# Performance work log

Measured on AMD Instinct MI355X. Metric: run time of the kernel, lower is better.

## Reference

```python
import jax, jax.numpy as jnp
import numpy as np

EPS = 1e-12


def setup_inputs() -> dict:
    key = jax.random.key(0)
    k1, k2 = jax.random.split(key)
    ide_feats = jax.random.normal(k1, (4096, 256), dtype=jnp.float32)
    u_feats = jax.random.normal(k2, (16384, 256), dtype=jnp.float32)
    return {"ide_feats": ide_feats, "u_feats": u_feats}


def reference(ide_feats, u_feats):
    # euclidean_dist: sqrt(sum((x_i - y_j)^2) + eps) -> [N, M]
    # computed via the GEMM expansion to avoid the [N, M, D] intermediate
    x2 = jnp.sum(ide_feats * ide_feats, axis=-1)[:, None]   # [N, 1]
    y2 = jnp.sum(u_feats * u_feats, axis=-1)[None, :]       # [1, M]
    xy = jnp.einsum('nd,md->nm', ide_feats, u_feats)        # [N, M]
    d2 = jnp.maximum(x2 + y2 - 2.0 * xy, 0.0)
    dists = jnp.sqrt(d2 + EPS)                              # [N, M]
    d = jnp.mean(dists, axis=-1)                            # [N]
    # dist_loss: sum_{i,j} sqrt((d_i - d_j)^2 + eps)
    diff = d[:, None] - d[None, :]                          # [N, N]
    loss = jnp.sum(jnp.sqrt(diff * diff + EPS))
    return loss
```

## Files before the change

kernel.cpp:

```cpp
#include <hip/hip_runtime.h>
#include <hip/hip_bf16.h>
#include <cstdint>

#define N_IDE 4096
#define M_U   16384
#define D_DIM 256
#define EPSF  1e-12f
#define INV_M (1.0f / 16384.0f)

#define CGC   512
#define BK    32
#define SB_ELEMS (CGC * BK)

typedef _Float16 f16x8 __attribute__((ext_vector_type(8)));
typedef float    f32x4 __attribute__((ext_vector_type(4)));

__device__ __forceinline__ void gll16(const void* g, void* l) {
  __builtin_amdgcn_global_load_lds(
      (const __attribute__((address_space(1))) void*)(uintptr_t)g,
      (__attribute__((address_space(3))) void*)(uint32_t)(uintptr_t)l,
      16, 0, 0);
}

__device__ __forceinline__ unsigned short f2h_bits(float f) {
  _Float16 h = (_Float16)f;
  return __builtin_bit_cast(unsigned short, h);
}

__global__ __launch_bounds__(256) void k_conv(const float* __restrict__ ide,
                                              const float* __restrict__ u,
                                              unsigned short* __restrict__ Ah,
                                              unsigned short* __restrict__ Bh,
                                              float* __restrict__ x2,
                                              float* __restrict__ y2) {
  int gw = (blockIdx.x * 256 + threadIdx.x) >> 6;
  int l  = threadIdx.x & 63;
  const float4* src;
  ushort4* dst;
  float* nrm;
  if (gw < N_IDE) {
    src = (const float4*)(ide + (size_t)gw * D_DIM);
    dst = (ushort4*)(Ah + (size_t)gw * D_DIM);
    nrm = x2 + gw;
  } else {
    int r = gw - N_IDE;
    src = (const float4*)(u + (size_t)r * D_DIM);
    dst = (ushort4*)(Bh + (size_t)r * D_DIM);
    nrm = y2 + r;
  }
  float4 v = src[l];
  float s = v.x * v.x + v.y * v.y + v.z * v.z + v.w * v.w;
  ushort4 o;
  o.x = f2h_bits(v.x); o.y = f2h_bits(v.y);
  o.z = f2h_bits(v.z); o.w = f2h_bits(v.w);
  dst[l] = o;
#pragma unroll
  for (int m = 1; m <= 32; m <<= 1) s += __shfl_xor(s, m, 64);
  if (l == 0) *nrm = s;
}

__global__ __launch_bounds__(512, 2) void k_gemm(const unsigned short* __restrict__ Ah,
                                                 const unsigned short* __restrict__ Bh,
                                                 const float* __restrict__ x2,
                                                 const float* __restrict__ y2,
                                                 float* __restrict__ partial) {
  __shared__ __align__(16) unsigned short sA[128 * 256];
  __shared__ __align__(16) unsigned short sB[2 * SB_ELEMS];
  __shared__ float rowacc[4][128];

  const int t    = threadIdx.x;
  const int w    = t >> 6;
  const int l    = t & 63;
  const int wm   = w >> 2, wn = w & 3;
  const int lrow = l & 15;
  const int lhi  = l >> 4;
  const int bx   = blockIdx.x;
  const int by   = blockIdx.y;

  rowacc[t >> 7][t & 127] = 0.f;

#pragma unroll
  for (int i = 0; i < 8; ++i) {
    int L = i * 512 + t;
    int row = L >> 5;
    int p = L & 31;
    int c = (p & 24) | ((p & 7) ^ (row & 7));
    gll16(Ah + (size_t)(by * 128 + row) * D_DIM + c * 8,
          sA + (size_t)(i * 512 + w * 64) * 8);
  }

  auto stageB = [&](int s) {
    const int cgi = (s >> 3) * 8 + bx;
    const int kt  = s & 7;
    const unsigned short* src = Bh + (size_t)cgi * CGC * D_DIM + kt * BK;
    unsigned short* dstb = sB + (size_t)(s & 1) * SB_ELEMS;
#pragma unroll
    for (int j = 0; j < 4; ++j) {
      int L = j * 512 + t;
      int row = L >> 2;
      int c = L & 3;
      gll16(src + (size_t)row * D_DIM + c * 8,
            dstb + (size_t)(j * 512 + w * 64) * 8);
    }
  };

  float4 x2v[4];
#pragma unroll
  for (int mi = 0; mi < 4; ++mi)
    x2v[mi] = *(const float4*)&x2[by * 128 + wm * 64 + mi * 16 + lhi * 4];

  stageB(0);
  __syncthreads();

  for (int cg = 0; cg < 4; ++cg) {
    const int cgi = cg * 8 + bx;

    f32x4 acc[4][8];
#pragma unroll
    for (int mi = 0; mi < 4; ++mi)
#pragma unroll
      for (int ni = 0; ni < 8; ++ni)
        acc[mi][ni] = (f32x4){0.f, 0.f, 0.f, 0.f};

    for (int kt = 0; kt < 8; ++kt) {
      const int s = cg * 8 + kt;
      if (s + 1 < 32) stageB(s + 1);

      f16x8 af[4];
#pragma unroll
      for (int mi = 0; mi < 4; ++mi) {
        int arow = wm * 64 + mi * 16 + lrow;
        int lc   = kt * 4 + lhi;
        int pc   = (lc & 24) | ((lc & 7) ^ (lrow & 7));
        af[mi] = *(const f16x8*)(sA + (size_t)arow * 256 + pc * 8);
      }

      const unsigned short* bbuf = sB + (size_t)(s & 1) * SB_ELEMS;
#pragma unroll
      for (int half = 0; half < 2; ++half) {
        f16x8 bf[4];
#pragma unroll
        for (int nj = 0; nj < 4; ++nj) {
          int brow = wn * 128 + (half * 4 + nj) * 16 + lrow;
          bf[nj] = *(const f16x8*)(bbuf + (size_t)brow * BK + lhi * 8);
        }
#pragma unroll
        for (int mi = 0; mi < 4; ++mi)
#pragma unroll
          for (int nj = 0; nj < 4; ++nj)
            acc[mi][half * 4 + nj] =
                __builtin_amdgcn_mfma_f32_16x16x32_f16(af[mi], bf[nj],
                                                       acc[mi][half * 4 + nj], 0, 0, 0);
      }
      __syncthreads();
    }

    float yv[8];
#pragma unroll
    for (int ni = 0; ni < 8; ++ni)
      yv[ni] = y2[cgi * CGC + wn * 128 + ni * 16 + lrow];

#pragma unroll
    for (int mi = 0; mi < 4; ++mi) {
      float xr[4] = {x2v[mi].x, x2v[mi].y, x2v[mi].z, x2v[mi].w};
#pragma unroll
      for (int rr = 0; rr < 4; ++rr) {
        float ssum = 0.f;
#pragma unroll
        for (int ni = 0; ni < 8; ++ni) {
          float d2 = xr[rr] + yv[ni] - 2.0f * acc[mi][ni][rr];
          d2 = fmaxf(d2, 0.0f);
          ssum += __builtin_amdgcn_sqrtf(d2 + EPSF);
        }
        ssum += __shfl_xor(ssum, 1, 64);
        ssum += __shfl_xor(ssum, 2, 64);
        ssum += __shfl_xor(ssum, 4, 64);
        ssum += __shfl_xor(ssum, 8, 64);
        if (lrow == 0)
          rowacc[wn][wm * 64 + mi * 16 + lhi * 4 + rr] += ssum;
      }
    }
  }

  __syncthreads();
  if (t < 128)
    partial[(size_t)bx * N_IDE + by * 128 + t] =
        rowacc[0][t] + rowacc[1][t] + rowacc[2][t] + rowacc[3][t];
}

__global__ __launch_bounds__(256) void k_loss(const float* __restrict__ partial,
                                              float* __restrict__ out) {
  __shared__ float sd[N_IDE];
  __shared__ float wsum[4];
  int t = threadIdx.x;
  for (int k = t; k < N_IDE; k += 256) {
    float s = 0.f;
#pragma unroll
    for (int b = 0; b < 8; ++b) s += partial[(size_t)b * N_IDE + k];
    sd[k] = s;
  }
  __syncthreads();
  int tid = blockIdx.x * 256 + t;
  int i   = tid >> 4;
  int jl  = tid & 15;
  float di = sd[i];
  float s  = 0.f;
  for (int k = 0; k < 256; ++k) {
    float diff = (di - sd[jl + k * 16]) * INV_M;
    s += __builtin_amdgcn_sqrtf(diff * diff + EPSF);
  }
#pragma unroll
  for (int m = 1; m <= 32; m <<= 1) s += __shfl_xor(s, m, 64);
  if ((t & 63) == 0) wsum[t >> 6] = s;
  __syncthreads();
  if (t == 0) atomicAdd(out, wsum[0] + wsum[1] + wsum[2] + wsum[3]);
}

extern "C" void kernel_launch(void* const* d_in, const int* in_sizes, int n_in,
                              void* d_out, int out_size, void* d_ws, size_t ws_size,
                              hipStream_t stream) {
  (void)in_sizes; (void)n_in; (void)out_size; (void)ws_size;
  const float* ide = (const float*)d_in[0];
  const float* u   = (const float*)d_in[1];
  float* out = (float*)d_out;

  char* ws = (char*)d_ws;
  size_t off = 0;
  unsigned short* Ah = (unsigned short*)(ws + off); off += (size_t)N_IDE * D_DIM * 2;
  unsigned short* Bh = (unsigned short*)(ws + off); off += (size_t)M_U  * D_DIM * 2;
  float* x2      = (float*)(ws + off); off += (size_t)N_IDE * 4;
  float* y2      = (float*)(ws + off); off += (size_t)M_U * 4;
  float* partial = (float*)(ws + off); off += (size_t)8 * N_IDE * 4;

  hipMemsetAsync(d_out, 0, sizeof(float), stream);
  k_conv<<<(N_IDE + M_U) / 4, 256, 0, stream>>>(ide, u, Ah, Bh, x2, y2);
  k_gemm<<<dim3(8, 32), 512, 0, stream>>>(Ah, Bh, x2, y2, partial);
  k_loss<<<256, 256, 0, stream>>>(partial, out);
}
```

Baseline: 127.8 us.

## Deepen B-tile pipeline to four buffers with swizzled LDS and register row sums

The GEMM kernel's column chunk shrinks from 512 to 256, and B staging moves from double buffering to a 4-deep ring with three tiles in flight. Explicit vmcnt waits plus raw s_barrier replace __syncthreads, and the B LDS layout gets an XOR swizzle to cut bank conflicts. y2 is preloaded into LDS, and row sums stay in registers and are written as 32 partial slots instead of passing through a shared rowacc. This is meant to hide global load latency, reduce accumulator register pressure and remove LDS reduction traffic. In exchange k_loss must sum four times more partials, and the hand-written waitcnt logic is fragile.

```diff
diff --git a/kernel.cpp b/kernel.cpp
--- a/kernel.cpp
+++ b/kernel.cpp
@@ -8,9 +8,11 @@
 #define EPSF  1e-12f
 #define INV_M (1.0f / 16384.0f)
 
-#define CGC   512
+#define CGC   256
 #define BK    32
 #define SB_ELEMS (CGC * BK)
+#define NBUF  4
+#define NSTEP 64
 
 typedef _Float16 f16x8 __attribute__((ext_vector_type(8)));
 typedef float    f32x4 __attribute__((ext_vector_type(4)));
@@ -65,8 +67,8 @@
                                                  const float* __restrict__ y2,
                                                  float* __restrict__ partial) {
   __shared__ __align__(16) unsigned short sA[128 * 256];
-  __shared__ __align__(16) unsigned short sB[2 * SB_ELEMS];
-  __shared__ float rowacc[4][128];
+  __shared__ __align__(16) unsigned short sB[NBUF * SB_ELEMS];
+  __shared__ __align__(16) float sY[8 * CGC];
 
   const int t    = threadIdx.x;
   const int w    = t >> 6;
@@ -76,8 +78,12 @@
   const int lhi  = l >> 4;
   const int bx   = blockIdx.x;
   const int by   = blockIdx.y;
-
-  rowacc[t >> 7][t & 127] = 0.f;
+  const int pchB = lhi ^ ((lrow >> 1) & 3);
+
+  float4 x2v[4];
+#pragma unroll
+  for (int mi = 0; mi < 4; ++mi)
+    x2v[mi] = *(const float4*)&x2[by * 128 + wm * 64 + mi * 16 + lhi * 4];
 
 #pragma unroll
   for (int i = 0; i < 8; ++i) {
@@ -88,104 +94,116 @@
     gll16(Ah + (size_t)(by * 128 + row) * D_DIM + c * 8,
           sA + (size_t)(i * 512 + w * 64) * 8);
   }
+  gll16(y2 + (size_t)(w * 8 + bx) * CGC + l * 4, sY + w * CGC + l * 4);
+
+  const int r0 = t >> 2,        r1 = (512 + t) >> 2;
+  const int c0 = (t & 3) ^ ((r0 >> 1) & 3);
+  const int c1 = (t & 3) ^ ((r1 >> 1) & 3);
+  const size_t soff0 = (size_t)r0 * D_DIM + c0 * 8;
+  const size_t soff1 = (size_t)r1 * D_DIM + c1 * 8;
 
   auto stageB = [&](int s) {
-    const int cgi = (s >> 3) * 8 + bx;
-    const int kt  = s & 7;
-    const unsigned short* src = Bh + (size_t)cgi * CGC * D_DIM + kt * BK;
-    unsigned short* dstb = sB + (size_t)(s & 1) * SB_ELEMS;
-#pragma unroll
-    for (int j = 0; j < 4; ++j) {
-      int L = j * 512 + t;
-      int row = L >> 2;
-      int c = L & 3;
-      gll16(src + (size_t)row * D_DIM + c * 8,
-            dstb + (size_t)(j * 512 + w * 64) * 8);
+    const unsigned short* src =
+        Bh + (size_t)(((s >> 3) * 8 + bx) * CGC) * D_DIM + (s & 7) * BK;
+    unsigned short* dstb = sB + (size_t)(s & 3) * SB_ELEMS;
+    gll16(src + soff0, dstb + (size_t)(w * 64) * 8);
+    gll16(src + soff1, dstb + (size_t)(512 + w * 64) * 8);
+  };
+
+  stageB(0); stageB(1); stageB(2);
+  asm volatile("s_waitcnt vmcnt(4)" ::: "memory");
+  asm volatile("s_barrier" ::: "memory");
+
+  f32x4 acc[4][4];
+#pragma unroll
+  for (int mi = 0; mi < 4; ++mi)
+#pragma unroll
+    for (int nj = 0; nj < 4; ++nj)
+      acc[mi][nj] = (f32x4){0.f, 0.f, 0.f, 0.f};
+
+  float racc[4][4];
+#pragma unroll
+  for (int mi = 0; mi < 4; ++mi)
+#pragma unroll
+    for (int rr = 0; rr < 4; ++rr)
+      racc[mi][rr] = 0.f;
+
+  for (int s = 0; s < NSTEP; ++s) {
+    const int kt = s & 7;
+    if (s + 3 < NSTEP) stageB(s + 3);
+
+    const int lc = kt * 4 + lhi;
+    const int pc = (lc & 24) | ((lc & 7) ^ (lrow & 7));
+    f16x8 af[4];
+#pragma unroll
+    for (int mi = 0; mi < 4; ++mi)
+      af[mi] = *(const f16x8*)(sA + (size_t)(wm * 64 + mi * 16 + lrow) * 256 + pc * 8);
+
+    const unsigned short* bbuf = sB + (size_t)(s & 3) * SB_ELEMS;
+    f16x8 bf[4];
+#pragma unroll
+    for (int nj = 0; nj < 4; ++nj)
+      bf[nj] = *(const f16x8*)(bbuf + (size_t)(wn * 64 + nj * 16 + lrow) * BK + pchB * 8);
+
+#pragma unroll
+    for (int mi = 0; mi < 4; ++mi)
+#pragma unroll
+      for (int nj = 0; nj < 4; ++nj)
+        acc[mi][nj] = __builtin_amdgcn_mfma_f32_16x16x32_f16(af[mi], bf[nj],
+                                                             acc[mi][nj], 0, 0, 0);
+
+    if (kt == 7) {
+      const int cgl = s >> 3;
+      float yv[4];
+#pragma unroll
+      for (int ni = 0; ni < 4; ++ni)
+        yv[ni] = sY[cgl * CGC + wn * 64 + ni * 16 + lrow];
+#pragma unroll
+      for (int mi = 0; mi < 4; ++mi) {
+        float xr[4] = {x2v[mi].x, x2v[mi].y, x2v[mi].z, x2v[mi].w};
+#pragma unroll
+        for (int rr = 0; rr < 4; ++rr) {
+          float ssum = 0.f;
+#pragma unroll
+          for (int ni = 0; ni < 4; ++ni) {
+            float d2 = xr[rr] + yv[ni] - 2.0f * acc[mi][ni][rr];
+            d2 = fmaxf(d2, 0.0f);
+            ssum += __builtin_amdgcn_sqrtf(d2 + EPSF);
+          }
+          racc[mi][rr] += ssum;
+        }
+      }
+#pragma unroll
+      for (int mi = 0; mi < 4; ++mi)
+#pragma unroll
+        for (int nj = 0; nj < 4; ++nj)
+          acc[mi][nj] = (f32x4){0.f, 0.f, 0.f, 0.f};
     }
-  };
-
-  float4 x2v[4];
-#pragma unroll
-  for (int mi = 0; mi < 4; ++mi)
-    x2v[mi] = *(const float4*)&x2[by * 128 + wm * 64 + mi * 16 + lhi * 4];
-
-  stageB(0);
-  __syncthreads();
-
-  for (int cg = 0; cg < 4; ++cg) {
-    const int cgi = cg * 8 + bx;
-
-    f32x4 acc[4][8];
-#pragma unroll
-    for (int mi = 0; mi < 4; ++mi)
-#pragma unroll
-      for (int ni = 0; ni < 8; ++ni)
-        acc[mi][ni] = (f32x4){0.f, 0.f, 0.f, 0.f};
-
-    for (int kt = 0; kt < 8; ++kt) {
-      const int s = cg * 8 + kt;
-      if (s + 1 < 32) stageB(s + 1);
-
-      f16x8 af[4];
-#pragma unroll
-      for (int mi = 0; mi < 4; ++mi) {
-        int arow = wm * 64 + mi * 16 + lrow;
-        int lc   = kt * 4 + lhi;
-        int pc   = (lc & 24) | ((lc & 7) ^ (lrow & 7));
-        af[mi] = *(const f16x8*)(sA + (size_t)arow * 256 + pc * 8);
-      }
-
-      const unsigned short* bbuf = sB + (size_t)(s & 1) * SB_ELEMS;
-#pragma unroll
-      for (int half = 0; half < 2; ++half) {
-        f16x8 bf[4];
-#pragma unroll
-        for (int nj = 0; nj < 4; ++nj) {
-          int brow = wn * 128 + (half * 4 + nj) * 16 + lrow;
-          bf[nj] = *(const f16x8*)(bbuf + (size_t)brow * BK + lhi * 8);
-        }
-#pragma unroll
-        for (int mi = 0; mi < 4; ++mi)
-#pragma unroll
-          for (int nj = 0; nj < 4; ++nj)
-            acc[mi][half * 4 + nj] =
-                __builtin_amdgcn_mfma_f32_16x16x32_f16(af[mi], bf[nj],
-                                                       acc[mi][half * 4 + nj], 0, 0, 0);
-      }
-      __syncthreads();
+
+    if (s < NSTEP - 3)       asm volatile("s_waitcnt vmcnt(4)" ::: "memory");
+    else if (s == NSTEP - 3) asm volatile("s_waitcnt vmcnt(2)" ::: "memory");
+    else                     asm volatile("s_waitcnt vmcnt(0)" ::: "memory");
+    asm volatile("s_barrier" ::: "memory");
+  }
+
+  const int slot = bx * 4 + wn;
+#pragma unroll
+  for (int mi = 0; mi < 4; ++mi) {
+    float rv[4];
+#pragma unroll
+    for (int rr = 0; rr < 4; ++rr) {
+      float v = racc[mi][rr];
+      v += __shfl_xor(v, 1, 64);
+      v += __shfl_xor(v, 2, 64);
+      v += __shfl_xor(v, 4, 64);
+      v += __shfl_xor(v, 8, 64);
+      rv[rr] = v;
     }
-
-    float yv[8];
-#pragma unroll
-    for (int ni = 0; ni < 8; ++ni)
-      yv[ni] = y2[cgi * CGC + wn * 128 + ni * 16 + lrow];
-
-#pragma unroll
-    for (int mi = 0; mi < 4; ++mi) {
-      float xr[4] = {x2v[mi].x, x2v[mi].y, x2v[mi].z, x2v[mi].w};
-#pragma unroll
-      for (int rr = 0; rr < 4; ++rr) {
-        float ssum = 0.f;
-#pragma unroll
-        for (int ni = 0; ni < 8; ++ni) {
-          float d2 = xr[rr] + yv[ni] - 2.0f * acc[mi][ni][rr];
-          d2 = fmaxf(d2, 0.0f);
-          ssum += __builtin_amdgcn_sqrtf(d2 + EPSF);
-        }
-        ssum += __shfl_xor(ssum, 1, 64);
-        ssum += __shfl_xor(ssum, 2, 64);
-        ssum += __shfl_xor(ssum, 4, 64);
-        ssum += __shfl_xor(ssum, 8, 64);
-        if (lrow == 0)
-          rowacc[wn][wm * 64 + mi * 16 + lhi * 4 + rr] += ssum;
-      }
+    if (lrow == 0) {
+      float4 o = make_float4(rv[0], rv[1], rv[2], rv[3]);
+      *(float4*)&partial[(size_t)slot * N_IDE + by * 128 + wm * 64 + mi * 16 + lhi * 4] = o;
     }
   }
-
-  __syncthreads();
-  if (t < 128)
-    partial[(size_t)bx * N_IDE + by * 128 + t] =
-        rowacc[0][t] + rowacc[1][t] + rowacc[2][t] + rowacc[3][t];
 }
 
 __global__ __launch_bounds__(256) void k_loss(const float* __restrict__ partial,
@@ -196,7 +214,7 @@
   for (int k = t; k < N_IDE; k += 256) {
     float s = 0.f;
 #pragma unroll
-    for (int b = 0; b < 8; ++b) s += partial[(size_t)b * N_IDE + k];
+    for (int b = 0; b < 32; ++b) s += partial[(size_t)b * N_IDE + k];
     sd[k] = s;
   }
   __syncthreads();
@@ -230,7 +248,7 @@
   unsigned short* Bh = (unsigned short*)(ws + off); off += (size_t)M_U  * D_DIM * 2;
   float* x2      = (float*)(ws + off); off += (size_t)N_IDE * 4;
   float* y2      = (float*)(ws + off); off += (size_t)M_U * 4;
-  float* partial = (float*)(ws + off); off += (size_t)8 * N_IDE * 4;
+  float* partial = (float*)(ws + off); off += (size_t)32 * N_IDE * 4;
 
   hipMemsetAsync(d_out, 0, sizeof(float), stream);
   k_conv<<<(N_IDE + M_U) / 4, 256, 0, stream>>>(ide, u, Ah, Bh, x2, y2);
```

Measured after the change: 137.0 us. +7.2%, slower.

## Restructure distance GEMM: more blocks, B fragments loaded straight from global into registers

Applied to the files above, without the earlier changes.

The GEMM grid grows from 8x32 to 32x32 blocks, and each block now covers a single 128x512 tile instead of looping over four column groups. B operands are no longer staged through double-buffered LDS. Each wave reads its B fragments directly from global memory into registers, double-buffered across k, and handles 128 rows by 64 columns. This is meant to raise parallelism and remove the LDS staging and per-k barriers, but uncoalesced global reads of B may cost bandwidth. A separate k_dsum kernel now reduces the 32 partial buffers before the loss kernel.

```diff
diff --git a/kernel.cpp b/kernel.cpp
--- a/kernel.cpp
+++ b/kernel.cpp
@@ -7,10 +7,6 @@
 #define D_DIM 256
 #define EPSF  1e-12f
 #define INV_M (1.0f / 16384.0f)
-
-#define CGC   512
-#define BK    32
-#define SB_ELEMS (CGC * BK)
 
 typedef _Float16 f16x8 __attribute__((ext_vector_type(8)));
 typedef float    f32x4 __attribute__((ext_vector_type(4)));
@@ -65,19 +61,15 @@
                                                  const float* __restrict__ y2,
                                                  float* __restrict__ partial) {
   __shared__ __align__(16) unsigned short sA[128 * 256];
-  __shared__ __align__(16) unsigned short sB[2 * SB_ELEMS];
-  __shared__ float rowacc[4][128];
+  __shared__ float rowacc[8][128];
 
   const int t    = threadIdx.x;
   const int w    = t >> 6;
   const int l    = t & 63;
-  const int wm   = w >> 2, wn = w & 3;
   const int lrow = l & 15;
   const int lhi  = l >> 4;
   const int bx   = blockIdx.x;
   const int by   = blockIdx.y;
-
-  rowacc[t >> 7][t & 127] = 0.f;
 
 #pragma unroll
   for (int i = 0; i < 8; ++i) {
@@ -88,117 +80,99 @@
     gll16(Ah + (size_t)(by * 128 + row) * D_DIM + c * 8,
           sA + (size_t)(i * 512 + w * 64) * 8);
   }
-
-  auto stageB = [&](int s) {
-    const int cgi = (s >> 3) * 8 + bx;
-    const int kt  = s & 7;
-    const unsigned short* src = Bh + (size_t)cgi * CGC * D_DIM + kt * BK;
-    unsigned short* dstb = sB + (size_t)(s & 1) * SB_ELEMS;
-#pragma unroll
-    for (int j = 0; j < 4; ++j) {
-      int L = j * 512 + t;
-      int row = L >> 2;
-      int c = L & 3;
-      gll16(src + (size_t)row * D_DIM + c * 8,
-            dstb + (size_t)(j * 512 + w * 64) * 8);
+  __syncthreads();
+
+  const int colbase = bx * 512 + w * 64;
+
+  const unsigned short* bptr[4];
+#pragma unroll
+  for (int nj = 0; nj < 4; ++nj)
+    bptr[nj] = Bh + (size_t)(colbase + nj * 16 + lrow) * D_DIM + lhi * 8;
+
+  f32x4 acc[8][4];
+#pragma unroll
+  for (int mi = 0; mi < 8; ++mi)
+#pragma unroll
+    for (int nj = 0; nj < 4; ++nj)
+      acc[mi][nj] = (f32x4){0.f, 0.f, 0.f, 0.f};
+
+  f16x8 bfb[2][4];
+#pragma unroll
+  for (int nj = 0; nj < 4; ++nj) bfb[0][nj] = *(const f16x8*)(bptr[nj]);
+
+#pragma unroll
+  for (int kt = 0; kt < 8; ++kt) {
+    if (kt < 7) {
+#pragma unroll
+      for (int nj = 0; nj < 4; ++nj)
+        bfb[(kt + 1) & 1][nj] = *(const f16x8*)(bptr[nj] + (kt + 1) * 32);
     }
-  };
-
-  float4 x2v[4];
-#pragma unroll
-  for (int mi = 0; mi < 4; ++mi)
-    x2v[mi] = *(const float4*)&x2[by * 128 + wm * 64 + mi * 16 + lhi * 4];
-
-  stageB(0);
-  __syncthreads();
-
-  for (int cg = 0; cg < 4; ++cg) {
-    const int cgi = cg * 8 + bx;
-
-    f32x4 acc[4][8];
-#pragma unroll
-    for (int mi = 0; mi < 4; ++mi)
-#pragma unroll
-      for (int ni = 0; ni < 8; ++ni)
-        acc[mi][ni] = (f32x4){0.f, 0.f, 0.f, 0.f};
-
-    for (int kt = 0; kt < 8; ++kt) {
-      const int s = cg * 8 + kt;
-      if (s + 1 < 32) stageB(s + 1);
-
-      f16x8 af[4];
-#pragma unroll
-      for (int mi = 0; mi < 4; ++mi) {
-        int arow = wm * 64 + mi * 16 + lrow;
-        int lc   = kt * 4 + lhi;
-        int pc   = (lc & 24) | ((lc & 7) ^ (lrow & 7));
-        af[mi] = *(const f16x8*)(sA + (size_t)arow * 256 + pc * 8);
+    const int lc = kt * 4 + lhi;
+    const int pc = (lc & 24) | ((lc & 7) ^ (lrow & 7));
+    f16x8 af[8];
+#pragma unroll
+    for (int mi = 0; mi < 8; ++mi)
+      af[mi] = *(const f16x8*)(sA + (size_t)(mi * 16 + lrow) * 256 + pc * 8);
+#pragma unroll
+    for (int mi = 0; mi < 8; ++mi)
+#pragma unroll
+      for (int nj = 0; nj < 4; ++nj)
+        acc[mi][nj] = __builtin_amdgcn_mfma_f32_16x16x32_f16(af[mi], bfb[kt & 1][nj],
+                                                             acc[mi][nj], 0, 0, 0);
+  }
+
+  float yv[4];
+#pragma unroll
+  for (int nj = 0; nj < 4; ++nj) yv[nj] = y2[colbase + nj * 16 + lrow];
+
+#pragma unroll
+  for (int mi = 0; mi < 8; ++mi) {
+    float4 x2v = *(const float4*)&x2[by * 128 + mi * 16 + lhi * 4];
+    float xr[4] = {x2v.x, x2v.y, x2v.z, x2v.w};
+    float rv[4];
+#pragma unroll
+    for (int rr = 0; rr < 4; ++rr) {
+      float ssum = 0.f;
+#pragma unroll
+      for (int nj = 0; nj < 4; ++nj) {
+        float d2 = xr[rr] + yv[nj] - 2.0f * acc[mi][nj][rr];
+        d2 = fmaxf(d2, 0.0f);
+        ssum += __builtin_amdgcn_sqrtf(d2 + EPSF);
       }
-
-      const unsigned short* bbuf = sB + (size_t)(s & 1) * SB_ELEMS;
-#pragma unroll
-      for (int half = 0; half < 2; ++half) {
-        f16x8 bf[4];
-#pragma unroll
-        for (int nj = 0; nj < 4; ++nj) {
-          int brow = wn * 128 + (half * 4 + nj) * 16 + lrow;
-          bf[nj] = *(const f16x8*)(bbuf + (size_t)brow * BK + lhi * 8);
-        }
-#pragma unroll
-        for (int mi = 0; mi < 4; ++mi)
-#pragma unroll
-          for (int nj = 0; nj < 4; ++nj)
-            acc[mi][half * 4 + nj] =
-                __builtin_amdgcn_mfma_f32_16x16x32_f16(af[mi], bf[nj],
-                                                       acc[mi][half * 4 + nj], 0, 0, 0);
-      }
-      __syncthreads();
+      ssum += __shfl_xor(ssum, 1, 64);
+      ssum += __shfl_xor(ssum, 2, 64);
+      ssum += __shfl_xor(ssum, 4, 64);
+      ssum += __shfl_xor(ssum, 8, 64);
+      rv[rr] = ssum;
     }
-
-    float yv[8];
-#pragma unroll
-    for (int ni = 0; ni < 8; ++ni)
-      yv[ni] = y2[cgi * CGC + wn * 128 + ni * 16 + lrow];
-
-#pragma unroll
-    for (int mi = 0; mi < 4; ++mi) {
-      float xr[4] = {x2v[mi].x, x2v[mi].y, x2v[mi].z, x2v[mi].w};
-#pragma unroll
-      for (int rr = 0; rr < 4; ++rr) {
-        float ssum = 0.f;
-#pragma unroll
-        for (int ni = 0; ni < 8; ++ni) {
-          float d2 = xr[rr] + yv[ni] - 2.0f * acc[mi][ni][rr];
-          d2 = fmaxf(d2, 0.0f);
-          ssum += __builtin_amdgcn_sqrtf(d2 + EPSF);
-        }
-        ssum += __shfl_xor(ssum, 1, 64);
-        ssum += __shfl_xor(ssum, 2, 64);
-        ssum += __shfl_xor(ssum, 4, 64);
-        ssum += __shfl_xor(ssum, 8, 64);
-        if (lrow == 0)
-          rowacc[wn][wm * 64 + mi * 16 + lhi * 4 + rr] += ssum;
-      }
-    }
-  }
-
-  __syncthreads();
-  if (t < 128)
-    partial[(size_t)bx * N_IDE + by * 128 + t] =
-        rowacc[0][t] + rowacc[1][t] + rowacc[2][t] + rowacc[3][t];
-}
-
-__global__ __launch_bounds__(256) void k_loss(const float* __restrict__ partial,
+    if (lrow == 0)
+      *(float4*)&rowacc[w][mi * 16 + lhi * 4] = make_float4(rv[0], rv[1], rv[2], rv[3]);
+  }
+
+  __syncthreads();
+  if (t < 128) {
+    float s = 0.f;
+#pragma unroll
+    for (int ww = 0; ww < 8; ++ww) s += rowacc[ww][t];
+    partial[(size_t)bx * N_IDE + by * 128 + t] = s;
+  }
+}
+
+__global__ __launch_bounds__(256) void k_dsum(const float* __restrict__ partial,
+                                              float* __restrict__ d) {
+  int k = blockIdx.x * 256 + threadIdx.x;
+  float s = 0.f;
+#pragma unroll
+  for (int b = 0; b < 32; ++b) s += partial[(size_t)b * N_IDE + k];
+  d[k] = s;
+}
+
+__global__ __launch_bounds__(256) void k_loss(const float* __restrict__ d,
                                               float* __restrict__ out) {
   __shared__ float sd[N_IDE];
   __shared__ float wsum[4];
   int t = threadIdx.x;
-  for (int k = t; k < N_IDE; k += 256) {
-    float s = 0.f;
-#pragma unroll
-    for (int b = 0; b < 8; ++b) s += partial[(size_t)b * N_IDE + k];
-    sd[k] = s;
-  }
+  for (int k = t; k < N_IDE; k += 256) sd[k] = d[k];
   __syncthreads();
   int tid = blockIdx.x * 256 + t;
   int i   = tid >> 4;
@@ -230,10 +204,12 @@
   unsigned short* Bh = (unsigned short*)(ws + off); off += (size_t)M_U  * D_DIM * 2;
   float* x2      = (float*)(ws + off); off += (size_t)N_IDE * 4;
   float* y2      = (float*)(ws + off); off += (size_t)M_U * 4;
-  float* partial = (float*)(ws + off); off += (size_t)8 * N_IDE * 4;
+  float* partial = (float*)(ws + off); off += (size_t)32 * N_IDE * 4;
+  float* dvec    = (float*)(ws + off); off += (size_t)N_IDE * 4;
 
   hipMemsetAsync(d_out, 0, sizeof(float), stream);
   k_conv<<<(N_IDE + M_U) / 4, 256, 0, stream>>>(ide, u, Ah, Bh, x2, y2);
-  k_gemm<<<dim3(8, 32), 512, 0, stream>>>(Ah, Bh, x2, y2, partial);
-  k_loss<<<256, 256, 0, stream>>>(partial, out);
-}
+  k_gemm<<<dim3(32, 32), 512, 0, stream>>>(Ah, Bh, x2, y2, partial);
+  k_dsum<<<N_IDE / 256, 256, 0, stream>>>(partial, dvec);
+  k_loss<<<256, 256, 0, stream>>>(dvec, out);
+}
```

Measured after the change: 141.2 us. +10.4%, slower.
